# Kernel tuning notes

Hardware: AMD Instinct MI355X
Metric: run time of the kernel (lower is better)

## Reference

```python
import jax, jax.numpy as jnp
import numpy as np

IN_FEATURES = 8192
OUT_FEATURES = 8192
MAX_STATES = 100
THRESHOLD = MAX_STATES // 2  # 50


def setup_inputs() -> dict:
    key = jax.random.key(0)
    k1, k2 = jax.random.split(key)
    # synapse_states ~ Normal(threshold-5, 3), clamped to [1, max_states]
    states = THRESHOLD - 5.0 + 3.0 * jax.random.normal(k1, (OUT_FEATURES, IN_FEATURES), dtype=jnp.float32)
    states = jnp.clip(states, 1.0, float(MAX_STATES))
    spike_input = (jax.random.uniform(k2, (IN_FEATURES,), dtype=jnp.float32) < 0.2).astype(jnp.float32)
    return {
        'spike_input': spike_input,
        'synapse_states': states,
        'membrane_potential': jnp.zeros((OUT_FEATURES,), dtype=jnp.float32),
        'adaptive_threshold': jnp.full((OUT_FEATURES,), 4.0, dtype=jnp.float32),
        'eligibility_trace': jnp.zeros((OUT_FEATURES, IN_FEATURES), dtype=jnp.float32),
    }


def reference(spike_input, synapse_states, membrane_potential, adaptive_threshold, eligibility_trace):
    # ternary (here effectively binary) weights from synapse states
    w = (synapse_states > float(THRESHOLD)).astype(jnp.float32)          # [O, I]
    x = spike_input                                                       # [I]
    conn_sum = jnp.maximum(jnp.sum(w, axis=1), 5.0)                       # [O]
    current = (w @ x) * (15.0 / jnp.sqrt(conn_sum))                       # [O]
    v_mem = membrane_potential * 0.85 + current                           # leaky integrate
    spikes = (v_mem >= adaptive_threshold).astype(jnp.float32)            # fire
    # eligibility trace update: decay + outer(spikes, x), clamped to [0, 5]
    new_trace = jnp.clip(eligibility_trace * 0.9 + jnp.outer(spikes, x), 0.0, 5.0)
    # adaptive threshold update, clamped to [2, 15]
    new_threshold = jnp.clip(adaptive_threshold + (spikes - 0.1) * 0.1, 2.0, 15.0)
    # soft reset of membrane potential
    new_v_mem = v_mem * (1.0 - spikes) * 0.1
    return spikes, new_v_mem, new_threshold, new_trace
```

## Files before the change

kernel.cpp:

```cpp
#include <hip/hip_runtime.h>

#define IN_F 8192
#define OUT_F 8192

typedef float v4f __attribute__((ext_vector_type(4)));

__global__ __launch_bounds__(256) void snn_fused_kernel(
    const float* __restrict__ x,
    const float* __restrict__ states,
    const float* __restrict__ mp,
    const float* __restrict__ thr,
    const float* __restrict__ trace,
    float* __restrict__ out)
{
    const int o = blockIdx.x;
    const int t = threadIdx.x;

    __shared__ float red_ws[4];
    __shared__ float red_dot[4];

    const float mp_o  = mp[o];
    const float thr_o = thr[o];

    const v4f* __restrict__ x4  = (const v4f*)x;
    const v4f* __restrict__ s4  = (const v4f*)(states + (size_t)o * IN_F);
    const v4f* __restrict__ tr4 = (const v4f*)(trace  + (size_t)o * IN_F);

    v4f xr[8], tr[8];
    float wsum = 0.0f, dot = 0.0f;
#pragma unroll
    for (int k = 0; k < 8; ++k) {
        const int idx = t + (k << 8);
        xr[k] = x4[idx];
        tr[k] = __builtin_nontemporal_load(&tr4[idx]);
        const v4f sv = __builtin_nontemporal_load(&s4[idx]);
        const float w0 = (sv[0] > 50.0f) ? 1.0f : 0.0f;
        const float w1 = (sv[1] > 50.0f) ? 1.0f : 0.0f;
        const float w2 = (sv[2] > 50.0f) ? 1.0f : 0.0f;
        const float w3 = (sv[3] > 50.0f) ? 1.0f : 0.0f;
        wsum += (w0 + w1) + (w2 + w3);
        dot  += (w0 * xr[k][0] + w1 * xr[k][1]) + (w2 * xr[k][2] + w3 * xr[k][3]);
    }

#pragma unroll
    for (int off = 32; off > 0; off >>= 1) {
        wsum += __shfl_down(wsum, off);
        dot  += __shfl_down(dot,  off);
    }
    const int wave = t >> 6;
    if ((t & 63) == 0) { red_ws[wave] = wsum; red_dot[wave] = dot; }
    __syncthreads();

    const float ws = (red_ws[0] + red_ws[1]) + (red_ws[2] + red_ws[3]);
    const float dt = (red_dot[0] + red_dot[1]) + (red_dot[2] + red_dot[3]);
    const float conn    = fmaxf(ws, 5.0f);
    const float current = dt * (15.0f / sqrtf(conn));
    const float v       = mp_o * 0.85f + current;
    const float spike   = (v >= thr_o) ? 1.0f : 0.0f;

    if (t == 0) {
        out[o]             = spike;
        out[OUT_F + o]     = v * (1.0f - spike) * 0.1f;
        out[2 * OUT_F + o] = fminf(fmaxf(thr_o + (spike - 0.1f) * 0.1f, 2.0f), 15.0f);
    }

    v4f* __restrict__ ot4 = (v4f*)(out + 3 * OUT_F + (size_t)o * IN_F);
#pragma unroll
    for (int k = 0; k < 8; ++k) {
        const int idx = t + (k << 8);
        v4f r;
        r[0] = fminf(fmaxf(tr[k][0] * 0.9f + spike * xr[k][0], 0.0f), 5.0f);
        r[1] = fminf(fmaxf(tr[k][1] * 0.9f + spike * xr[k][1], 0.0f), 5.0f);
        r[2] = fminf(fmaxf(tr[k][2] * 0.9f + spike * xr[k][2], 0.0f), 5.0f);
        r[3] = fminf(fmaxf(tr[k][3] * 0.9f + spike * xr[k][3], 0.0f), 5.0f);
        __builtin_nontemporal_store(r, &ot4[idx]);
    }
}

extern "C" void kernel_launch(void* const* d_in, const int* in_sizes, int n_in,
                              void* d_out, int out_size, void* d_ws, size_t ws_size,
                              hipStream_t stream) {
    const float* x      = (const float*)d_in[0];
    const float* states = (const float*)d_in[1];
    const float* mp     = (const float*)d_in[2];
    const float* thr    = (const float*)d_in[3];
    const float* trace  = (const float*)d_in[4];
    float* out = (float*)d_out;

    snn_fused_kernel<<<OUT_F, 256, 0, stream>>>(x, states, mp, thr, trace, out);
}
```

Baseline: 560.9 us.

## Map one output row per wavefront and defer trace loads until after spike

Each 64-lane wavefront now processes a whole output row, and a block covers four rows. This replaces the block-wide shared-memory reduction and __syncthreads with an xor-shuffle reduction inside the wave. Trace loads no longer sit in registers during the reduction; they are issued after the spike is known and interleaved with re-reading x. The aim is to cut synchronisation and register pressure so occupancy rises, at the cost of serialising the trace read behind the states read within each wave and reloading x.

```diff
diff --git a/kernel.cpp b/kernel.cpp
--- a/kernel.cpp
+++ b/kernel.cpp
@@ -2,6 +2,7 @@
 
 #define IN_F 8192
 #define OUT_F 8192
+#define NF4 (IN_F / 4)
 
 typedef float v4f __attribute__((ext_vector_type(4)));
 
@@ -13,66 +14,59 @@
     const float* __restrict__ trace,
     float* __restrict__ out)
 {
-    const int o = blockIdx.x;
-    const int t = threadIdx.x;
-
-    __shared__ float red_ws[4];
-    __shared__ float red_dot[4];
+    const int wave = threadIdx.x >> 6;
+    const int lane = threadIdx.x & 63;
+    const int o    = (blockIdx.x << 2) + wave;
 
     const float mp_o  = mp[o];
     const float thr_o = thr[o];
 
-    const v4f* __restrict__ x4  = (const v4f*)x;
-    const v4f* __restrict__ s4  = (const v4f*)(states + (size_t)o * IN_F);
-    const v4f* __restrict__ tr4 = (const v4f*)(trace  + (size_t)o * IN_F);
+    const v4f* __restrict__ x4 = (const v4f*)x;
+    const v4f* __restrict__ s4 = (const v4f*)(states + (size_t)o * IN_F);
 
-    v4f xr[8], tr[8];
     float wsum = 0.0f, dot = 0.0f;
-#pragma unroll
-    for (int k = 0; k < 8; ++k) {
-        const int idx = t + (k << 8);
-        xr[k] = x4[idx];
-        tr[k] = __builtin_nontemporal_load(&tr4[idx]);
+#pragma unroll 8
+    for (int k = 0; k < 32; ++k) {
+        const int idx = lane + (k << 6);
         const v4f sv = __builtin_nontemporal_load(&s4[idx]);
+        const v4f xv = x4[idx];
         const float w0 = (sv[0] > 50.0f) ? 1.0f : 0.0f;
         const float w1 = (sv[1] > 50.0f) ? 1.0f : 0.0f;
         const float w2 = (sv[2] > 50.0f) ? 1.0f : 0.0f;
         const float w3 = (sv[3] > 50.0f) ? 1.0f : 0.0f;
         wsum += (w0 + w1) + (w2 + w3);
-        dot  += (w0 * xr[k][0] + w1 * xr[k][1]) + (w2 * xr[k][2] + w3 * xr[k][3]);
+        dot  += (w0 * xv[0] + w1 * xv[1]) + (w2 * xv[2] + w3 * xv[3]);
     }
 
 #pragma unroll
-    for (int off = 32; off > 0; off >>= 1) {
-        wsum += __shfl_down(wsum, off);
-        dot  += __shfl_down(dot,  off);
+    for (int off = 1; off < 64; off <<= 1) {
+        wsum += __shfl_xor(wsum, off);
+        dot  += __shfl_xor(dot,  off);
     }
-    const int wave = t >> 6;
-    if ((t & 63) == 0) { red_ws[wave] = wsum; red_dot[wave] = dot; }
-    __syncthreads();
 
-    const float ws = (red_ws[0] + red_ws[1]) + (red_ws[2] + red_ws[3]);
-    const float dt = (red_dot[0] + red_dot[1]) + (red_dot[2] + red_dot[3]);
-    const float conn    = fmaxf(ws, 5.0f);
-    const float current = dt * (15.0f / sqrtf(conn));
+    const float conn    = fmaxf(wsum, 5.0f);
+    const float current = dot * (15.0f / sqrtf(conn));
     const float v       = mp_o * 0.85f + current;
     const float spike   = (v >= thr_o) ? 1.0f : 0.0f;
 
-    if (t == 0) {
+    if (lane == 0) {
         out[o]             = spike;
         out[OUT_F + o]     = v * (1.0f - spike) * 0.1f;
         out[2 * OUT_F + o] = fminf(fmaxf(thr_o + (spike - 0.1f) * 0.1f, 2.0f), 15.0f);
     }
 
-    v4f* __restrict__ ot4 = (v4f*)(out + 3 * OUT_F + (size_t)o * IN_F);
-#pragma unroll
-    for (int k = 0; k < 8; ++k) {
-        const int idx = t + (k << 8);
+    const v4f* __restrict__ tr4 = (const v4f*)(trace + (size_t)o * IN_F);
+    v4f* __restrict__       ot4 = (v4f*)(out + 3 * OUT_F + (size_t)o * IN_F);
+#pragma unroll 8
+    for (int k = 0; k < 32; ++k) {
+        const int idx = lane + (k << 6);
+        const v4f tv = __builtin_nontemporal_load(&tr4[idx]);
+        const v4f xv = x4[idx];
         v4f r;
-        r[0] = fminf(fmaxf(tr[k][0] * 0.9f + spike * xr[k][0], 0.0f), 5.0f);
-        r[1] = fminf(fmaxf(tr[k][1] * 0.9f + spike * xr[k][1], 0.0f), 5.0f);
-        r[2] = fminf(fmaxf(tr[k][2] * 0.9f + spike * xr[k][2], 0.0f), 5.0f);
-        r[3] = fminf(fmaxf(tr[k][3] * 0.9f + spike * xr[k][3], 0.0f), 5.0f);
+        r[0] = fminf(fmaxf(tv[0] * 0.9f + spike * xv[0], 0.0f), 5.0f);
+        r[1] = fminf(fmaxf(tv[1] * 0.9f + spike * xv[1], 0.0f), 5.0f);
+        r[2] = fminf(fmaxf(tv[2] * 0.9f + spike * xv[2], 0.0f), 5.0f);
+        r[3] = fminf(fmaxf(tv[3] * 0.9f + spike * xv[3], 0.0f), 5.0f);
         __builtin_nontemporal_store(r, &ot4[idx]);
     }
 }
@@ -87,5 +81,5 @@
     const float* trace  = (const float*)d_in[4];
     float* out = (float*)d_out;
 
-    snn_fused_kernel<<<OUT_F, 256, 0, stream>>>(x, states, mp, thr, trace, out);
+    snn_fused_kernel<<<OUT_F / 4, 256, 0, stream>>>(x, states, mp, thr, trace, out);
 }
```

New measurement: 570.3 us. About the same (+1.7%).

## Split fused SNN kernel into separate spike and trace-update kernels

Applied to the files above, without the earlier changes.

Splits the single fused kernel into two launches. The first computes the weighted dot product, spikes, membrane and threshold per row. The second is a flat elementwise kernel that updates the eligibility trace using the spikes already written to the output. This removes the per-row dependency that held the trace tile in registers across the reduction and barrier, and lets the trace stream run as a simple fully parallel pass. In exchange it adds a second launch and a serialization point, and the trace kernel still reads the full trace once and writes it once.

```diff
diff --git a/kernel.cpp b/kernel.cpp
--- a/kernel.cpp
+++ b/kernel.cpp
@@ -5,12 +5,11 @@
 
 typedef float v4f __attribute__((ext_vector_type(4)));
 
-__global__ __launch_bounds__(256) void snn_fused_kernel(
+__global__ __launch_bounds__(256) void spike_kernel(
     const float* __restrict__ x,
     const float* __restrict__ states,
     const float* __restrict__ mp,
     const float* __restrict__ thr,
-    const float* __restrict__ trace,
     float* __restrict__ out)
 {
     const int o = blockIdx.x;
@@ -22,24 +21,21 @@
     const float mp_o  = mp[o];
     const float thr_o = thr[o];
 
-    const v4f* __restrict__ x4  = (const v4f*)x;
-    const v4f* __restrict__ s4  = (const v4f*)(states + (size_t)o * IN_F);
-    const v4f* __restrict__ tr4 = (const v4f*)(trace  + (size_t)o * IN_F);
+    const v4f* __restrict__ x4 = (const v4f*)x;
+    const v4f* __restrict__ s4 = (const v4f*)(states + (size_t)o * IN_F);
 
-    v4f xr[8], tr[8];
     float wsum = 0.0f, dot = 0.0f;
 #pragma unroll
     for (int k = 0; k < 8; ++k) {
         const int idx = t + (k << 8);
-        xr[k] = x4[idx];
-        tr[k] = __builtin_nontemporal_load(&tr4[idx]);
         const v4f sv = __builtin_nontemporal_load(&s4[idx]);
+        const v4f xv = x4[idx];
         const float w0 = (sv[0] > 50.0f) ? 1.0f : 0.0f;
         const float w1 = (sv[1] > 50.0f) ? 1.0f : 0.0f;
         const float w2 = (sv[2] > 50.0f) ? 1.0f : 0.0f;
         const float w3 = (sv[3] > 50.0f) ? 1.0f : 0.0f;
         wsum += (w0 + w1) + (w2 + w3);
-        dot  += (w0 * xr[k][0] + w1 * xr[k][1]) + (w2 * xr[k][2] + w3 * xr[k][3]);
+        dot  += (w0 * xv[0] + w1 * xv[1]) + (w2 * xv[2] + w3 * xv[3]);
     }
 
 #pragma unroll
@@ -51,28 +47,42 @@
     if ((t & 63) == 0) { red_ws[wave] = wsum; red_dot[wave] = dot; }
     __syncthreads();
 
-    const float ws = (red_ws[0] + red_ws[1]) + (red_ws[2] + red_ws[3]);
-    const float dt = (red_dot[0] + red_dot[1]) + (red_dot[2] + red_dot[3]);
-    const float conn    = fmaxf(ws, 5.0f);
-    const float current = dt * (15.0f / sqrtf(conn));
-    const float v       = mp_o * 0.85f + current;
-    const float spike   = (v >= thr_o) ? 1.0f : 0.0f;
-
     if (t == 0) {
+        const float ws = (red_ws[0] + red_ws[1]) + (red_ws[2] + red_ws[3]);
+        const float dt = (red_dot[0] + red_dot[1]) + (red_dot[2] + red_dot[3]);
+        const float conn    = fmaxf(ws, 5.0f);
+        const float current = dt * (15.0f / sqrtf(conn));
+        const float v       = mp_o * 0.85f + current;
+        const float spike   = (v >= thr_o) ? 1.0f : 0.0f;
         out[o]             = spike;
         out[OUT_F + o]     = v * (1.0f - spike) * 0.1f;
         out[2 * OUT_F + o] = fminf(fmaxf(thr_o + (spike - 0.1f) * 0.1f, 2.0f), 15.0f);
     }
+}
 
-    v4f* __restrict__ ot4 = (v4f*)(out + 3 * OUT_F + (size_t)o * IN_F);
+__global__ __launch_bounds__(256) void trace_kernel(
+    const float* __restrict__ x,
+    const float* __restrict__ trace,
+    const float* __restrict__ spikes,
+    float* __restrict__ otrace)
+{
+    const int tid = blockIdx.x * 256 + threadIdx.x;
+    const v4f* __restrict__ x4  = (const v4f*)x;
+    const v4f* __restrict__ tr4 = (const v4f*)trace;
+    v4f* __restrict__       ot4 = (v4f*)otrace;
+
 #pragma unroll
     for (int k = 0; k < 8; ++k) {
-        const int idx = t + (k << 8);
+        const int idx = tid + k * (8192 * 256);
+        const int row = idx >> 11;
+        const float s = spikes[row];
+        const v4f tv = __builtin_nontemporal_load(&tr4[idx]);
+        const v4f xv = x4[idx & 2047];
         v4f r;
-        r[0] = fminf(fmaxf(tr[k][0] * 0.9f + spike * xr[k][0], 0.0f), 5.0f);
-        r[1] = fminf(fmaxf(tr[k][1] * 0.9f + spike * xr[k][1], 0.0f), 5.0f);
-        r[2] = fminf(fmaxf(tr[k][2] * 0.9f + spike * xr[k][2], 0.0f), 5.0f);
-        r[3] = fminf(fmaxf(tr[k][3] * 0.9f + spike * xr[k][3], 0.0f), 5.0f);
+        r[0] = fminf(fmaxf(tv[0] * 0.9f + s * xv[0], 0.0f), 5.0f);
+        r[1] = fminf(fmaxf(tv[1] * 0.9f + s * xv[1], 0.0f), 5.0f);
+        r[2] = fminf(fmaxf(tv[2] * 0.9f + s * xv[2], 0.0f), 5.0f);
+        r[3] = fminf(fmaxf(tv[3] * 0.9f + s * xv[3], 0.0f), 5.0f);
         __builtin_nontemporal_store(r, &ot4[idx]);
     }
 }
@@ -87,5 +97,6 @@
     const float* trace  = (const float*)d_in[4];
     float* out = (float*)d_out;
 
-    snn_fused_kernel<<<OUT_F, 256, 0, stream>>>(x, states, mp, thr, trace, out);
+    spike_kernel<<<OUT_F, 256, 0, stream>>>(x, states, mp, thr, out);
+    trace_kernel<<<8192, 256, 0, stream>>>(x, trace, out, out + 3 * OUT_F);
 }
```

Measured after the change: 567.1 us. About the same (+1.1%).
